# Performance work log

Measured on AMD Instinct MI355X. Metric: run time of the kernel, lower is better.

The kernel has to match this reference:

```python
import jax, jax.numpy as jnp
import numpy as np

BATCH, IN_SIZE, CH, DIM, MODES, LAYERS, PROJ, OUT = 16, 1, 128, 128, 32, 4, 128, 1


def setup_inputs() -> dict:
    key = jax.random.key(0)
    ks = jax.random.split(key, 12)
    scale = 1.0 / (CH * CH)
    inp = {
        "z": jax.random.normal(ks[0], (BATCH, IN_SIZE, DIM, DIM), dtype=jnp.float32),
        # Lifting: pointwise linear input_size -> channels
        "lift_w": jax.random.normal(ks[1], (CH, IN_SIZE), dtype=jnp.float32) / np.sqrt(IN_SIZE),
        "lift_b": jnp.zeros((CH,), dtype=jnp.float32),
        # Spectral conv weights per layer, two mode corners, complex stored as real/imag
        "wr1": scale * jax.random.normal(ks[2], (LAYERS, CH, CH, MODES, MODES), dtype=jnp.float32),
        "wi1": scale * jax.random.normal(ks[3], (LAYERS, CH, CH, MODES, MODES), dtype=jnp.float32),
        "wr2": scale * jax.random.normal(ks[4], (LAYERS, CH, CH, MODES, MODES), dtype=jnp.float32),
        "wi2": scale * jax.random.normal(ks[5], (LAYERS, CH, CH, MODES, MODES), dtype=jnp.float32),
        # Projection: channels -> projection_size -> output_size (pointwise MLP)
        "pw1": jax.random.normal(ks[6], (PROJ, CH), dtype=jnp.float32) / np.sqrt(CH),
        "pb1": jnp.zeros((PROJ,), dtype=jnp.float32),
        "pw2": jax.random.normal(ks[7], (OUT, PROJ), dtype=jnp.float32) / np.sqrt(PROJ),
        "pb2": jnp.zeros((OUT,), dtype=jnp.float32),
    }
    return inp


def _spectral_conv(v, w1, w2, modes, size):
    # v: [b, c, X, Y] real; rfft2 over last two dims (norm='backward')
    vf = jnp.fft.rfft2(v, norm="backward")  # [b, c, X, Y//2+1] complex
    of = jnp.zeros_like(vf)
    # low-frequency corner
    of = of.at[:, :, :modes, :modes].set(
        jnp.einsum("bixy,ioxy->boxy", vf[:, :, :modes, :modes], w1))
    # high (negative) frequency corner along first spatial axis
    of = of.at[:, :, -modes:, :modes].set(
        jnp.einsum("bixy,ioxy->boxy", vf[:, :, -modes:, :modes], w2))
    return jnp.fft.irfft2(of, s=(size, size), norm="backward")


def reference(z, lift_w, lift_b, wr1, wi1, wr2, wi2, pw1, pb1, pw2, pb2):
    n_layers = wr1.shape[0]
    modes = wr1.shape[-1]
    size = z.shape[-1]
    # Lifting: [b, in, x, y] -> [b, ch, x, y]
    v = jnp.einsum("bixy,ci->bcxy", z, lift_w) + lift_b[None, :, None, None]
    out = v
    for l in range(n_layers):
        w1 = wr1[l] + 1j * wi1[l]
        w2 = wr2[l] + 1j * wi2[l]
        out = _spectral_conv(out, w1, w2, modes, size)
    # Projection MLP (pointwise over grid)
    h = jnp.einsum("bcxy,pc->bpxy", out, pw1) + pb1[None, :, None, None]
    h = jax.nn.gelu(h)
    out = jnp.einsum("bpxy,op->boxy", h, pw2) + pb2[None, :, None, None]
    return out
```

## Files before the change

kernel.cpp:

```cpp
#include <hip/hip_runtime.h>
#include <math.h>

#define B 16
#define CH 128
#define DIM 128
#define MODES 32
#define NLAYERS 4
#define PROJ 128
#define U 64
#define KY 32
#define NMODE (U*KY)
#define N2 (DIM*DIM)
#define PG 32
#define PPG (PROJ/PG)

__device__ __forceinline__ void async16(const void* g, void* l) {
  __builtin_amdgcn_global_load_lds((const __attribute__((address_space(1))) unsigned int*)g,
                                   (__attribute__((address_space(3))) unsigned int*)l, 16, 0, 0);
}

__global__ __launch_bounds__(256) void k_zf1(const float* __restrict__ z,
                                             float2* __restrict__ t1) {
  __shared__ float zrow[16][DIM];
  __shared__ float2 tw[DIM];
  int bid = blockIdx.x;
  int b = bid >> 3, xt = bid & 7;
  int x0 = xt * 16;
  int t = threadIdx.x;
  if (t < 128) {
    float ang = (float)(2.0 * M_PI) * (float)t / 128.0f;
    tw[t] = make_float2(cosf(ang), sinf(ang));
  }
  for (int e = t; e < 16 * DIM / 4; e += 256)
    ((float4*)&zrow[0][0])[e] = ((const float4*)&z[b * N2 + x0 * DIM])[e];
  __syncthreads();
  #pragma unroll
  for (int j = 0; j < 2; ++j) {
    int it = t + j * 256;
    int x_l = it >> 5, ky = it & 31;
    float tr = 0.f, ti = 0.f;
    for (int y = 0; y < DIM; ++y) {
      float v = zrow[x_l][y];
      float2 w = tw[(ky * y) & 127];
      tr += v * w.x;
      ti -= v * w.y;
    }
    t1[((size_t)b * DIM + x0 + x_l) * KY + ky] = make_float2(tr, ti);
  }
}

__global__ __launch_bounds__(256) void k_zf2(const float2* __restrict__ t1,
                                             float* __restrict__ zfr, float* __restrict__ zfi) {
  __shared__ float2 t1s[DIM][KY];
  __shared__ float2 tw[DIM];
  int bid = blockIdx.x;
  int b = bid >> 1, uh = bid & 1;
  int t = threadIdx.x;
  if (t < 128) {
    float ang = (float)(2.0 * M_PI) * (float)t / 128.0f;
    tw[t] = make_float2(cosf(ang), sinf(ang));
  }
  for (int e = t; e < DIM * KY / 2; e += 256)
    ((float4*)&t1s[0][0])[e] = ((const float4*)&t1[(size_t)b * DIM * KY])[e];
  __syncthreads();
  #pragma unroll
  for (int j = 0; j < 4; ++j) {
    int m = t + j * 256;
    int u_l = m >> 5, ky = m & 31;
    int u = uh * 32 + u_l;
    int kx = (u < 32) ? u : (u + 64);
    float ar = 0.f, ai = 0.f;
    for (int x = 0; x < DIM; ++x) {
      float2 v = t1s[x][ky];
      float2 w = tw[(kx * x) & 127];
      ar += v.x * w.x + v.y * w.y;
      ai += v.y * w.x - v.x * w.y;
    }
    zfr[b * NMODE + u * KY + ky] = ar;
    zfi[b * NMODE + u * KY + ky] = ai;
  }
}

__global__ __launch_bounds__(256) void k_lift(const float* __restrict__ zfr, const float* __restrict__ zfi,
                                              const float* __restrict__ lw, const float* __restrict__ lb,
                                              float2* __restrict__ vcout) {
  int idx = blockIdx.x * 256 + threadIdx.x;
  if (idx >= B * CH * NMODE) return;
  int m = idx & (NMODE - 1);
  int c = (idx >> 11) & 127;
  int b = idx >> 18;
  float w = lw[c];
  float re = w * zfr[b * NMODE + m];
  float im = w * zfi[b * NMODE + m];
  if (m == 0) re += 16384.f * lb[c];
  vcout[idx] = make_float2(re, im);
}

__global__ __launch_bounds__(256) void k_spec(const float2* __restrict__ vc,
                                              const float* __restrict__ wr1, const float* __restrict__ wi1,
                                              const float* __restrict__ wr2, const float* __restrict__ wi2,
                                              float2* __restrict__ oc) {
  __shared__ float4 ring[4][768];
  int bid = blockIdx.x;
  int u = ((bid & 7) << 3) | ((bid >> 3) & 7);
  int ot = bid >> 6;
  int o0 = ot * 8;
  int kxw = u & 31;
  const float* wr = (u >= 32) ? wr2 : wr1;
  const float* wi = (u >= 32) ? wi2 : wi1;
  int t = threadIdx.x;
  int ky = t & 31, bh = (t >> 5) & 1, oq = t >> 6;
  int wv = t >> 6, lane = t & 63;
  float accR[2][8] = {}, accI[2][8] = {};

  #define STAGE(c)                                                                   \
    if ((c) < 64) {                                                                  \
      char* dst0 = (char*)&ring[0][0] + (size_t)((c) & 3) * 12288;                   \
      int i0_ = (c) * 2;                                                             \
      _Pragma("unroll")                                                              \
      for (int n = 0; n < 3; ++n) {                                                  \
        int nu = wv * 3 + n;                                                         \
        if (nu < 4) {                                                                \
          int ri = nu >> 1, il = nu & 1;                                             \
          int o_l = lane >> 3, ky4 = (lane & 7) * 4;                                 \
          const float* src = (ri ? wi : wr) +                                        \
            (((size_t)(i0_ + il) * CH + o0 + o_l) * MODES + kxw) * MODES + ky4;      \
          async16(src, dst0 + nu * 1024 + lane * 16);                                \
        } else {                                                                     \
          int nv = nu - 4;                                                           \
          int il = nv >> 2;                                                          \
          int b_l = (nv & 3) * 4 + (lane >> 4), ky2 = (lane & 15) * 2;               \
          const float2* src = vc + ((size_t)b_l * CH + i0_ + il) * NMODE +           \
                              u * KY + ky2;                                          \
          async16(src, dst0 + 4096 + nv * 1024 + lane * 16);                         \
        }                                                                            \
      }                                                                              \
    }

  STAGE(0); STAGE(1); STAGE(2);
  for (int k = 0; k < 64; ++k) {
    __builtin_amdgcn_sched_barrier(0);
    if (k < 62)       asm volatile("s_waitcnt vmcnt(6)" ::: "memory");
    else if (k == 62) asm volatile("s_waitcnt vmcnt(3)" ::: "memory");
    else              asm volatile("s_waitcnt vmcnt(0)" ::: "memory");
    __builtin_amdgcn_s_barrier();
    __builtin_amdgcn_sched_barrier(0);
    STAGE(k + 3);
    {
      const char* dstc = (const char*)&ring[0][0] + (size_t)(k & 3) * 12288;
      const float*  Wb = (const float*)dstc;
      const float2* Vb = (const float2*)(dstc + 4096);
      #pragma unroll
      for (int il = 0; il < 2; ++il) {
        float wrv[2], wiv[2];
        #pragma unroll
        for (int j = 0; j < 2; ++j) {
          wrv[j] = Wb[il * 256 + (oq * 2 + j) * 32 + ky];
          wiv[j] = Wb[(2 + il) * 256 + (oq * 2 + j) * 32 + ky];
        }
        #pragma unroll
        for (int bb = 0; bb < 8; ++bb) {
          int b = bh * 8 + bb;
          float2 v = Vb[il * 512 + (b >> 2) * 128 + (b & 3) * 32 + ky];
          #pragma unroll
          for (int j = 0; j < 2; ++j) {
            accR[j][bb] += wrv[j] * v.x - wiv[j] * v.y;
            accI[j][bb] += wrv[j] * v.y + wiv[j] * v.x;
          }
        }
      }
    }
  }
  #undef STAGE
  #pragma unroll
  for (int j = 0; j < 2; ++j)
    #pragma unroll
    for (int bb = 0; bb < 8; ++bb) {
      int o = o0 + oq * 2 + j, b = bh * 8 + bb;
      oc[(((size_t)b * CH + o) * U + u) * KY + ky] = make_float2(accR[j][bb], accI[j][bb]);
    }
}

__global__ __launch_bounds__(256) void k_proj0(float2* __restrict__ vc) {
  int idx = blockIdx.x * 256 + threadIdx.x;
  if (idx >= B * CH * 33) return;
  int pi = idx % 33;
  int bc = idx / 33;
  float2* base = vc + (size_t)bc * NMODE;
  if (pi == 0) {
    base[0].y = 0.f;
  } else if (pi == 32) {
    base[32 * KY].x *= 0.5f;
    base[32 * KY].y *= 0.5f;
  } else {
    int ua = pi, ub = 64 - pi;
    float2 a = base[ua * KY], b2 = base[ub * KY];
    base[ua * KY] = make_float2(0.5f * (a.x + b2.x), 0.5f * (a.y - b2.y));
    base[ub * KY] = make_float2(0.5f * (b2.x + a.x), 0.5f * (b2.y - a.y));
  }
}

__global__ __launch_bounds__(256) void k_pw1(const float2* __restrict__ xc,
                                             const float* __restrict__ pw1,
                                             float2* __restrict__ hc) {
  __shared__ float wT[CH][CH + 1];
  int bid = blockIdx.x;
  int b = ((bid & 7) << 1) | ((bid >> 8) & 1);
  int jt = (bid >> 3) & 31;
  int t = threadIdx.x;
  for (int e = t; e < CH * CH; e += 256) {
    int p = e >> 7, c = e & 127;
    wT[c][p] = pw1[e];
  }
  __syncthreads();
  int tx = t & 15, ty = t >> 4;
  int j0 = jt * 64 + tx * 4;
  float accR[4][8] = {}, accI[4][8] = {};
  for (int c = 0; c < CH; ++c) {
    const float4* x4 = (const float4*)&xc[((size_t)b * CH + c) * NMODE + j0];
    float4 v0 = x4[0], v1 = x4[1];
    float xrv[4] = {v0.x, v0.z, v1.x, v1.z};
    float xiv[4] = {v0.y, v0.w, v1.y, v1.w};
    float w[8];
    #pragma unroll
    for (int pp = 0; pp < 8; ++pp) w[pp] = wT[c][ty * 8 + pp];
    #pragma unroll
    for (int jj = 0; jj < 4; ++jj)
      #pragma unroll
      for (int pp = 0; pp < 8; ++pp) {
        accR[jj][pp] += w[pp] * xrv[jj];
        accI[jj][pp] += w[pp] * xiv[jj];
      }
  }
  #pragma unroll
  for (int pp = 0; pp < 8; ++pp) {
    int p = ty * 8 + pp;
    float4* o4 = (float4*)&hc[((size_t)b * CH + p) * NMODE + j0];
    o4[0] = make_float4(accR[0][pp], accI[0][pp], accR[1][pp], accI[1][pp]);
    o4[1] = make_float4(accR[2][pp], accI[2][pp], accR[3][pp], accI[3][pp]);
  }
}

__global__ __launch_bounds__(256) void k_idft_partial(const float2* __restrict__ hc,
                                                      const float* __restrict__ pb1,
                                                      const float* __restrict__ pw2,
                                                      float* __restrict__ partial) {
  __shared__ float2 tw[DIM];
  __shared__ float2 hfs[2][NMODE];
  __shared__ float2 sbuf[16][KY];
  __shared__ float4 sE[8][32];
  int bid = blockIdx.x;
  int b = (bid & 7) | (((bid >> 3) & 1) << 3);
  int pg = (bid >> 4) & 31, xs = bid >> 9;
  int x0 = xs * 8;
  int t = threadIdx.x;
  int wv = t >> 6, lane = t & 63;
  if (t < 128) {
    float ang = (float)(2.0 * M_PI) * (float)t / 128.0f;
    tw[t] = make_float2(cosf(ang), sinf(ang));
  }

  #define STAGE_H(bf, pp_)                                                           \
    {                                                                                \
      const char* srcb = (const char*)(hc + ((size_t)b * CH + pg * PPG + (pp_)) * NMODE); \
      _Pragma("unroll")                                                              \
      for (int n = 0; n < 4; ++n) {                                                  \
        int nu = wv * 4 + n;                                                         \
        async16(srcb + (size_t)nu * 1024 + lane * 16,                                \
                (char*)&hfs[bf][0] + (size_t)nu * 1024 + lane * 16);                 \
      }                                                                              \
    }

  STAGE_H(0, 0);
  __syncthreads();
  {
    int xq = t >> 5, j = t & 31;
    int x = x0 + xq;
    int kxE = (j < 16) ? (2 * j) : (2 * j + 64);
    float2 wE = tw[(kxE * x) & 127];
    float2 wO = tw[((kxE + 1) * x) & 127];
    sE[xq][j] = make_float4(wE.x, wE.y, wO.x, wO.y);
  }
  int y = t & 63, xh = t >> 6;
  float Cr[KY], Sr[KY];
  #pragma unroll
  for (int ky = 0; ky < KY; ++ky) {
    float2 w = tw[(ky * y) & 127];
    float wk = (ky == 0) ? 1.f : 2.f;
    Cr[ky] = wk * w.x;
    Sr[ky] = -wk * w.y;
  }
  __syncthreads();
  int xqA = t >> 5, kyA = t & 31;
  float res[8] = {0.f, 0.f, 0.f, 0.f, 0.f, 0.f, 0.f, 0.f};
  for (int pp = 0; pp < PPG; ++pp) {
    int p = pg * PPG + pp;
    int cur = pp & 1;
    if (pp) __syncthreads();
    if (pp + 1 < PPG) STAGE_H(cur ^ 1, pp + 1);
    {
      float per = 0.f, pei = 0.f, por = 0.f, poi = 0.f;
      #pragma unroll
      for (int j = 0; j < 32; ++j) {
        float4 E = sE[xqA][j];
        float2 h0 = hfs[cur][(2 * j) * KY + kyA];
        float2 h1 = hfs[cur][(2 * j + 1) * KY + kyA];
        per += h0.x * E.x - h0.y * E.y;
        pei += h0.x * E.y + h0.y * E.x;
        por += h1.x * E.z - h1.y * E.w;
        poi += h1.x * E.w + h1.y * E.z;
      }
      sbuf[xqA][kyA]     = make_float2(per + por, pei + poi);
      sbuf[xqA + 8][kyA] = make_float2(per - por, pei - poi);
    }
    __syncthreads();
    float pb = pb1[p], pw = pw2[p];
    #pragma unroll
    for (int sl = 0; sl < 4; ++sl) {
      int s_i = xh + sl * 4;
      float ae = 0.f, ao = 0.f;
      #pragma unroll
      for (int ky = 0; ky < KY; ky += 2) {
        float4 v = *(const float4*)&sbuf[s_i][ky];
        ae += v.x * Cr[ky] + v.y * Sr[ky];
        ao += v.z * Cr[ky + 1] + v.w * Sr[ky + 1];
      }
      float hlo = (ae + ao) * (1.f / 16384.f) + pb;
      float hhi = (ae - ao) * (1.f / 16384.f) + pb;
      float zlo = 1.5957691216057308f * (hlo + 0.044715f * hlo * hlo * hlo);
      float zhi = 1.5957691216057308f * (hhi + 0.044715f * hhi * hhi * hhi);
      res[sl * 2]     += pw * hlo * __builtin_amdgcn_rcpf(1.f + __expf(-zlo));
      res[sl * 2 + 1] += pw * hhi * __builtin_amdgcn_rcpf(1.f + __expf(-zhi));
    }
  }
  #undef STAGE_H
  size_t pbase = ((size_t)pg * B + b) * N2;
  #pragma unroll
  for (int sl = 0; sl < 4; ++sl) {
    int s_i = xh + sl * 4;
    int x = x0 + (s_i & 7) + ((s_i >> 3) << 6);
    partial[pbase + x * DIM + y]      = res[sl * 2];
    partial[pbase + x * DIM + y + 64] = res[sl * 2 + 1];
  }
}

__global__ __launch_bounds__(256) void k_reduce(const float* __restrict__ partial,
                                                const float* __restrict__ pb2,
                                                float* __restrict__ outp) {
  int idx = blockIdx.x * 256 + threadIdx.x;
  if (idx >= B * N2) return;
  float s = pb2[0];
  #pragma unroll
  for (int pg = 0; pg < PG; ++pg) s += partial[(size_t)pg * B * N2 + idx];
  outp[idx] = s;
}

extern "C" void kernel_launch(void* const* d_in, const int* in_sizes, int n_in,
                              void* d_out, int out_size, void* d_ws, size_t ws_size,
                              hipStream_t stream) {
  const float* z   = (const float*)d_in[0];
  const float* lw  = (const float*)d_in[1];
  const float* lb  = (const float*)d_in[2];
  const float* wr1 = (const float*)d_in[3];
  const float* wi1 = (const float*)d_in[4];
  const float* wr2 = (const float*)d_in[5];
  const float* wi2 = (const float*)d_in[6];
  const float* pw1 = (const float*)d_in[7];
  const float* pb1 = (const float*)d_in[8];
  const float* pw2 = (const float*)d_in[9];
  const float* pb2 = (const float*)d_in[10];
  float* out = (float*)d_out;
  float* ws = (float*)d_ws;

  float* zfr = ws;
  float* zfi = zfr + 32768;
  float2* Ac = (float2*)(ws + 65536);
  float2* Bc = Ac + (size_t)B * CH * NMODE;
  float2* t1 = Bc;

  k_zf1<<<B * 8, 256, 0, stream>>>(z, t1);
  k_zf2<<<B * 2, 256, 0, stream>>>(t1, zfr, zfi);
  k_lift<<<(B * CH * NMODE) / 256, 256, 0, stream>>>(zfr, zfi, lw, lb, Ac);

  const size_t WSTRIDE = (size_t)CH * CH * MODES * MODES;
  float2 *ir = Ac, *oc = Bc;
  for (int l = 0; l < NLAYERS; ++l) {
    k_spec<<<1024, 256, 0, stream>>>(ir,
                                     wr1 + l * WSTRIDE, wi1 + l * WSTRIDE,
                                     wr2 + l * WSTRIDE, wi2 + l * WSTRIDE,
                                     oc);
    if (l < NLAYERS - 1)
      k_proj0<<<(B * CH * 33 + 255) / 256, 256, 0, stream>>>(oc);
    float2* tmp = ir; ir = oc; oc = tmp;
  }
  k_pw1<<<512, 256, 0, stream>>>(ir, pw1, oc);
  float* partial = (float*)ir;
  k_idft_partial<<<B * PG * 8, 256, 0, stream>>>(oc, pb1, pw2, partial);
  k_reduce<<<(B * N2) / 256, 256, 0, stream>>>(partial, pb2, out);
}
```

Measured before the change: 915.3 us.

## Enlarge spectral-conv tile to 32 outputs per block with 512 threads

```diff
diff --git a/kernel.cpp b/kernel.cpp
--- a/kernel.cpp
+++ b/kernel.cpp
@@ -96,74 +96,72 @@
   vcout[idx] = make_float2(re, im);
 }
 
-__global__ __launch_bounds__(256) void k_spec(const float2* __restrict__ vc,
+__global__ __launch_bounds__(512) void k_spec(const float2* __restrict__ vc,
                                               const float* __restrict__ wr1, const float* __restrict__ wi1,
                                               const float* __restrict__ wr2, const float* __restrict__ wi2,
                                               float2* __restrict__ oc) {
-  __shared__ float4 ring[4][768];
+  __shared__ float4 ring[3][3072];
   int bid = blockIdx.x;
   int u = ((bid & 7) << 3) | ((bid >> 3) & 7);
   int ot = bid >> 6;
-  int o0 = ot * 8;
+  int o0 = ot * 32;
   int kxw = u & 31;
   const float* wr = (u >= 32) ? wr2 : wr1;
   const float* wi = (u >= 32) ? wi2 : wi1;
   int t = threadIdx.x;
-  int ky = t & 31, bh = (t >> 5) & 1, oq = t >> 6;
+  int ky = t & 31, oh = (t >> 5) & 7, bh = t >> 8;
   int wv = t >> 6, lane = t & 63;
-  float accR[2][8] = {}, accI[2][8] = {};
+  float accR[4][8] = {}, accI[4][8] = {};
 
   #define STAGE(c)                                                                   \
-    if ((c) < 64) {                                                                  \
-      char* dst0 = (char*)&ring[0][0] + (size_t)((c) & 3) * 12288;                   \
-      int i0_ = (c) * 2;                                                             \
+    if ((c) < 32) {                                                                  \
+      char* dst0 = (char*)&ring[0][0] + (size_t)((c) % 3) * 49152;                   \
+      int i0_ = (c) * 4;                                                             \
       _Pragma("unroll")                                                              \
-      for (int n = 0; n < 3; ++n) {                                                  \
-        int nu = wv * 3 + n;                                                         \
-        if (nu < 4) {                                                                \
-          int ri = nu >> 1, il = nu & 1;                                             \
-          int o_l = lane >> 3, ky4 = (lane & 7) * 4;                                 \
+      for (int n = 0; n < 6; ++n) {                                                  \
+        int nu = wv * 6 + n;                                                         \
+        if (nu < 32) {                                                               \
+          int ri = nu >> 4, il = (nu >> 2) & 3, oo = nu & 3;                         \
+          int o_l = oo * 8 + (lane >> 3), ky4 = (lane & 7) * 4;                      \
           const float* src = (ri ? wi : wr) +                                        \
             (((size_t)(i0_ + il) * CH + o0 + o_l) * MODES + kxw) * MODES + ky4;      \
-          async16(src, dst0 + nu * 1024 + lane * 16);                                \
+          async16(src, dst0 + (size_t)nu * 1024 + lane * 16);                        \
         } else {                                                                     \
-          int nv = nu - 4;                                                           \
-          int il = nv >> 2;                                                          \
-          int b_l = (nv & 3) * 4 + (lane >> 4), ky2 = (lane & 15) * 2;               \
+          int nv = nu - 32;                                                          \
+          int il = nv >> 2, bq = nv & 3;                                             \
+          int b_l = bq * 4 + (lane >> 4), ky2 = (lane & 15) * 2;                     \
           const float2* src = vc + ((size_t)b_l * CH + i0_ + il) * NMODE +           \
                               u * KY + ky2;                                          \
-          async16(src, dst0 + 4096 + nv * 1024 + lane * 16);                         \
+          async16(src, dst0 + 32768 + (size_t)nv * 1024 + lane * 16);                \
         }                                                                            \
       }                                                                              \
     }
 
-  STAGE(0); STAGE(1); STAGE(2);
-  for (int k = 0; k < 64; ++k) {
+  STAGE(0); STAGE(1);
+  for (int k = 0; k < 32; ++k) {
     __builtin_amdgcn_sched_barrier(0);
-    if (k < 62)       asm volatile("s_waitcnt vmcnt(6)" ::: "memory");
-    else if (k == 62) asm volatile("s_waitcnt vmcnt(3)" ::: "memory");
-    else              asm volatile("s_waitcnt vmcnt(0)" ::: "memory");
+    if (k < 31) asm volatile("s_waitcnt vmcnt(6)" ::: "memory");
+    else        asm volatile("s_waitcnt vmcnt(0)" ::: "memory");
     __builtin_amdgcn_s_barrier();
     __builtin_amdgcn_sched_barrier(0);
-    STAGE(k + 3);
+    STAGE(k + 2);
     {
-      const char* dstc = (const char*)&ring[0][0] + (size_t)(k & 3) * 12288;
-      const float*  Wb = (const float*)dstc;
-      const float2* Vb = (const float2*)(dstc + 4096);
+      const char* slotc = (const char*)&ring[0][0] + (size_t)(k % 3) * 49152;
+      const float*  Wb = (const float*)slotc;
+      const float2* Vb = (const float2*)(slotc + 32768);
       #pragma unroll
-      for (int il = 0; il < 2; ++il) {
-        float wrv[2], wiv[2];
+      for (int il = 0; il < 4; ++il) {
+        float wrv[4], wiv[4];
         #pragma unroll
-        for (int j = 0; j < 2; ++j) {
-          wrv[j] = Wb[il * 256 + (oq * 2 + j) * 32 + ky];
-          wiv[j] = Wb[(2 + il) * 256 + (oq * 2 + j) * 32 + ky];
+        for (int j = 0; j < 4; ++j) {
+          wrv[j] = Wb[il * 1024 + (oh * 4 + j) * 32 + ky];
+          wiv[j] = Wb[4096 + il * 1024 + (oh * 4 + j) * 32 + ky];
         }
         #pragma unroll
         for (int bb = 0; bb < 8; ++bb) {
-          int b = bh * 8 + bb;
-          float2 v = Vb[il * 512 + (b >> 2) * 128 + (b & 3) * 32 + ky];
+          float2 v = Vb[il * 512 + (bh * 8 + bb) * 32 + ky];
           #pragma unroll
-          for (int j = 0; j < 2; ++j) {
+          for (int j = 0; j < 4; ++j) {
             accR[j][bb] += wrv[j] * v.x - wiv[j] * v.y;
             accI[j][bb] += wrv[j] * v.y + wiv[j] * v.x;
           }
@@ -173,10 +171,10 @@
   }
   #undef STAGE
   #pragma unroll
-  for (int j = 0; j < 2; ++j)
+  for (int j = 0; j < 4; ++j)
     #pragma unroll
     for (int bb = 0; bb < 8; ++bb) {
-      int o = o0 + oq * 2 + j, b = bh * 8 + bb;
+      int o = o0 + oh * 4 + j, b = bh * 8 + bb;
       oc[(((size_t)b * CH + o) * U + u) * KY + ky] = make_float2(accR[j][bb], accI[j][bb]);
     }
 }
@@ -385,10 +383,10 @@
   const size_t WSTRIDE = (size_t)CH * CH * MODES * MODES;
   float2 *ir = Ac, *oc = Bc;
   for (int l = 0; l < NLAYERS; ++l) {
-    k_spec<<<1024, 256, 0, stream>>>(ir,
-                                     wr1 + l * WSTRIDE, wi1 + l * WSTRIDE,
-                                     wr2 + l * WSTRIDE, wi2 + l * WSTRIDE,
-                                     oc);
+    k_spec<<<256, 512, 0, stream>>>(ir,
+                                    wr1 + l * WSTRIDE, wi1 + l * WSTRIDE,
+                                    wr2 + l * WSTRIDE, wi2 + l * WSTRIDE,
+                                    oc);
     if (l < NLAYERS - 1)
       k_proj0<<<(B * CH * 33 + 255) / 256, 256, 0, stream>>>(oc);
     float2* tmp = ir; ir = oc; oc = tmp;
```

Result: faster. 817.1 us (-10.7%).
